# Performance work log

Hardware: AMD Instinct MI355X
Metric: run time of the kernel (lower is better)

The kernel has to match this reference:

```python
import jax, jax.numpy as jnp
import numpy as np

C = 256
NUM_HEADS = 8
NUM_GROUPS = 32
EPS = 1e-5


def setup_inputs() -> dict:
    key = jax.random.key(0)
    ks = jax.random.split(key, 7)
    B, H, W = 2, 64, 64
    x = jax.random.normal(ks[0], (B, C, H, W), dtype=jnp.float32)
    norm_gamma = jnp.ones((C,), dtype=jnp.float32)
    norm_beta = jnp.zeros((C,), dtype=jnp.float32)
    # 1x1 convs == per-pixel linear layers; store weights as (out_ch, in_ch)
    qkv_w = jax.random.normal(ks[1], (3 * C, C), dtype=jnp.float32) * (1.0 / np.sqrt(C))
    qkv_b = jnp.zeros((3 * C,), dtype=jnp.float32)
    proj_w = jax.random.normal(ks[2], (C, C), dtype=jnp.float32) * (1.0 / np.sqrt(C))
    proj_b = jnp.zeros((C,), dtype=jnp.float32)
    return {"x": x, "norm_gamma": norm_gamma, "norm_beta": norm_beta,
            "qkv_w": qkv_w, "qkv_b": qkv_b, "proj_w": proj_w, "proj_b": proj_b}


def _group_norm(x, gamma, beta):
    B, Cc, H, W = x.shape
    xg = x.reshape(B, NUM_GROUPS, Cc // NUM_GROUPS, H, W)
    mean = xg.mean(axis=(2, 3, 4), keepdims=True)
    var = xg.var(axis=(2, 3, 4), keepdims=True)
    xn = ((xg - mean) * jax.lax.rsqrt(var + EPS)).reshape(B, Cc, H, W)
    return xn * gamma[None, :, None, None] + beta[None, :, None, None]


def reference(x, norm_gamma, norm_beta, qkv_w, qkv_b, proj_w, proj_b):
    B, Cc, H, W = x.shape
    hd = Cc // NUM_HEADS
    N = H * W

    h = _group_norm(x, norm_gamma, norm_beta)
    # 1x1 conv: (3C,C) x (B,C,H,W) -> (B,3C,H,W)
    qkv = jnp.einsum('oc,bchw->bohw', qkv_w, h) + qkv_b[None, :, None, None]
    q, k, v = jnp.split(qkv, 3, axis=1)

    def heads(t):  # (B,C,H,W) -> (B,heads,N,hd)
        return t.reshape(B, NUM_HEADS, hd, N).transpose(0, 1, 3, 2)

    q, k, v = heads(q), heads(k), heads(v)
    scale = hd ** (-0.5)
    attn = jax.nn.softmax(jnp.einsum('bhnd,bhmd->bhnm', q, k) * scale, axis=-1)
    out = jnp.einsum('bhnm,bhmd->bhnd', attn, v)  # (B,heads,N,hd)
    out = out.transpose(0, 1, 3, 2).reshape(B, Cc, H, W)
    out = jnp.einsum('oc,bchw->bohw', proj_w, out) + proj_b[None, :, None, None]
    return x + out
```

## Files before the change

### kernel.cpp

```cpp
#include <hip/hip_runtime.h>
#include <math.h>

#define C_    256
#define NH    8
#define HD_   32
#define NG    32
#define CPG   8
#define NPIX  4096
#define BATCH 2
#define EPSV  1e-5f
#define SLOG2 0.25503489f
#define MF    16.0f
#define KVB   64
#define KSTR  40
#define VSTR  72
#define KPS2  2048

typedef __bf16 bf16x8 __attribute__((ext_vector_type(8)));
typedef __bf16 bf16x4 __attribute__((ext_vector_type(4)));
typedef float  f32x4  __attribute__((ext_vector_type(4)));

__global__ __launch_bounds__(256) void prep_kernel(const float* __restrict__ x,
                                                   float* __restrict__ stats,
                                                   const float* __restrict__ qw,
                                                   const float* __restrict__ pw,
                                                   __bf16* __restrict__ wbq,
                                                   __bf16* __restrict__ wbp) {
    if (blockIdx.x >= 64) {
        const int i = ((blockIdx.x - 64) * 256 + threadIdx.x) * 4;
        const float* src;
        __bf16* dst;
        int off;
        if (i < 768 * 256) { src = qw; dst = wbq; off = i; }
        else { src = pw; dst = wbp; off = i - 768 * 256; }
        const float4 v = *(const float4*)(src + off);
        bf16x4 o;
        o[0] = (__bf16)v.x; o[1] = (__bf16)v.y; o[2] = (__bf16)v.z; o[3] = (__bf16)v.w;
        *(bf16x4*)(dst + off) = o;
        return;
    }
    const int blk = blockIdx.x;
    const int b = blk >> 5, g = blk & 31;
    const float* __restrict__ xp = x + ((size_t)(b * C_ + g * CPG)) * NPIX;

    float s = 0.f, ss = 0.f;
    for (int i = threadIdx.x * 4; i < CPG * NPIX; i += 256 * 4) {
        const float4 v = *(const float4*)(xp + i);
        s  += v.x + v.y + v.z + v.w;
        ss += v.x * v.x + v.y * v.y + v.z * v.z + v.w * v.w;
    }
    #pragma unroll
    for (int off = 32; off; off >>= 1) {
        s  += __shfl_down(s, off);
        ss += __shfl_down(ss, off);
    }
    __shared__ float ls[4], lss[4];
    const int wid = threadIdx.x >> 6, lane = threadIdx.x & 63;
    if (lane == 0) { ls[wid] = s; lss[wid] = ss; }
    __syncthreads();
    if (threadIdx.x == 0) {
        float S = 0.f, SS = 0.f;
        #pragma unroll
        for (int w = 0; w < 4; ++w) { S += ls[w]; SS += lss[w]; }
        const float inv_n = 1.0f / (float)(CPG * NPIX);
        const float mean = S * inv_n;
        const float var  = SS * inv_n - mean * mean;
        stats[blk * 2 + 0] = mean;
        stats[blk * 2 + 1] = rsqrtf(var + EPSV);
    }
}

__global__ __launch_bounds__(256) void qkv_gemm_kernel(const __bf16* __restrict__ wbq,
                                                       const float* __restrict__ bias,
                                                       const float* __restrict__ x,
                                                       const float* __restrict__ stats,
                                                       const float* __restrict__ gamma,
                                                       const float* __restrict__ beta,
                                                       __bf16* __restrict__ Qb,
                                                       __bf16* __restrict__ Kb,
                                                       __bf16* __restrict__ Vb) {
    const int b = blockIdx.z;
    const int n0 = blockIdx.x * 32;
    __shared__ __align__(16) __bf16 tile[32][264];

    {
        const int nn = (threadIdx.x & 7) * 4;
        const int cb = threadIdx.x >> 3;
        #pragma unroll
        for (int p = 0; p < 8; ++p) {
            const int c = cb + p * 32;
            const float4 v = *(const float4*)(x + ((size_t)(b * C_ + c)) * NPIX + n0 + nn);
            const int g = c >> 3;
            const float mean = stats[(b * NG + g) * 2 + 0];
            const float rstd = stats[(b * NG + g) * 2 + 1];
            const float ga = gamma[c] * rstd;
            const float be = beta[c] - mean * ga;
            tile[nn + 0][c] = (__bf16)(v.x * ga + be);
            tile[nn + 1][c] = (__bf16)(v.y * ga + be);
            tile[nn + 2][c] = (__bf16)(v.z * ga + be);
            tile[nn + 3][c] = (__bf16)(v.w * ga + be);
        }
    }
    __syncthreads();

    const int wave = threadIdx.x >> 6, lane = threadIdx.x & 63;
    const int col = lane & 15, g = lane >> 4;
    const int m0 = blockIdx.y * 256 + wave * 64;

    f32x4 acc[4][2];
    #pragma unroll
    for (int i = 0; i < 4; ++i)
        #pragma unroll
        for (int j = 0; j < 2; ++j) acc[i][j] = (f32x4){0.f, 0.f, 0.f, 0.f};

    #pragma unroll
    for (int c0 = 0; c0 < C_; c0 += 32) {
        bf16x8 la[4], lb[2];
        #pragma unroll
        for (int mb = 0; mb < 4; ++mb)
            la[mb] = *(const bf16x8*)(wbq + (size_t)(m0 + mb * 16 + col) * C_ + c0 + g * 8);
        #pragma unroll
        for (int nb = 0; nb < 2; ++nb)
            lb[nb] = *(const bf16x8*)(&tile[nb * 16 + col][c0 + g * 8]);
        #pragma unroll
        for (int mb = 0; mb < 4; ++mb)
            #pragma unroll
            for (int nb = 0; nb < 2; ++nb)
                acc[mb][nb] = __builtin_amdgcn_mfma_f32_16x16x32_bf16(la[mb], lb[nb], acc[mb][nb], 0, 0, 0);
    }

    #pragma unroll
    for (int mb = 0; mb < 4; ++mb) {
        const int mbase = m0 + mb * 16 + 4 * g;
        const float4 b4 = *(const float4*)(bias + mbase);
        const int route = mbase >> 8;
        const int bh = b * NH + ((mbase >> 5) & 7);
        const int d0 = mbase & 31;
        #pragma unroll
        for (int nb = 0; nb < 2; ++nb) {
            const int n = n0 + nb * 16 + col;
            f32x4 v = acc[mb][nb];
            v[0] += b4.x; v[1] += b4.y; v[2] += b4.z; v[3] += b4.w;
            if (route == 0) {
                bf16x4 o;
                #pragma unroll
                for (int r = 0; r < 4; ++r) o[r] = (__bf16)(v[r] * SLOG2);
                *(bf16x4*)(Qb + (((size_t)bh * NPIX + n) << 5) + d0) = o;
            } else if (route == 1) {
                bf16x4 o;
                #pragma unroll
                for (int r = 0; r < 4; ++r) o[r] = (__bf16)v[r];
                *(bf16x4*)(Kb + (((size_t)bh * NPIX + n) << 5) + d0) = o;
            } else {
                #pragma unroll
                for (int r = 0; r < 4; ++r)
                    Vb[((size_t)bh * HD_ + d0 + r) * NPIX + n] = (__bf16)v[r];
            }
        }
    }
}

__global__ __launch_bounds__(512) void attn_kernel(const __bf16* __restrict__ Qb,
                                                   const __bf16* __restrict__ Kb,
                                                   const __bf16* __restrict__ Vb,
                                                   __bf16* __restrict__ aot) {
    __shared__ __align__(16) char smem[38912];
    __bf16 (*Ks)[2][KVB][KSTR] = (__bf16 (*)[2][KVB][KSTR])(smem);
    __bf16 (*Vs)[2][HD_][VSTR] = (__bf16 (*)[2][HD_][VSTR])(smem + 20480);
    float* pbuf = (float*)smem;

    const int id = blockIdx.x;
    const int h = id & 7;
    const int rest = id >> 3;
    const int b = rest >> 5;
    const int qt = rest & 31;

    const int wave = threadIdx.x >> 6, lane = threadIdx.x & 63;
    const int hw = wave >> 2, wv = wave & 3;
    const int col = lane & 15, g = lane >> 4;
    const int bh = b * NH + h;
    const int q0 = qt * 128 + wv * 32;

    const __bf16* __restrict__ qp = Qb + ((size_t)bh * NPIX + q0) * HD_;
    const __bf16* __restrict__ kp = Kb + ((size_t)bh * NPIX + hw * KPS2) * HD_;
    const __bf16* __restrict__ vp = Vb + (size_t)bh * HD_ * NPIX + hw * KPS2;

    const int sk_key = wv * 16 + (lane >> 2);
    const int sk_seg = (lane & 3) * 8;
    const int sv_d   = wv * 8 + (lane >> 3);
    const int sv_seg = (lane & 7) * 8;
    const int vslot  = (sv_seg & 32) + ((((sv_seg & 15) >> 2) << 3)) + (((sv_seg >> 4) & 1) << 2);
    const __bf16* __restrict__ kg = kp + (size_t)sk_key * HD_ + sk_seg;
    const __bf16* __restrict__ vg = vp + (size_t)sv_d * NPIX + sv_seg;

    const bf16x8 fq0 = *(const bf16x8*)(qp + col * HD_ + g * 8);
    const bf16x8 fq1 = *(const bf16x8*)(qp + (16 + col) * HD_ + g * 8);

    bf16x8 ones;
    #pragma unroll
    for (int j = 0; j < 8; ++j) ones[j] = (__bf16)1.0f;
    const f32x4 mfc = {-MF, -MF, -MF, -MF};

    f32x4 acc00 = {0.f,0.f,0.f,0.f}, acc01 = {0.f,0.f,0.f,0.f};
    f32x4 acc10 = {0.f,0.f,0.f,0.f}, acc11 = {0.f,0.f,0.f,0.f};
    f32x4 accL0 = {0.f,0.f,0.f,0.f}, accL1 = {0.f,0.f,0.f,0.f};

    {
        const bf16x8 rk = *(const bf16x8*)(kg);
        const bf16x8 rv = *(const bf16x8*)(vg);
        *(bf16x8*)&Ks[hw][0][sk_key][sk_seg] = rk;
        bf16x4 lo, hi;
        #pragma unroll
        for (int j = 0; j < 4; ++j) { lo[j] = rv[j]; hi[j] = rv[4 + j]; }
        *(bf16x4*)&Vs[hw][0][sv_d][vslot]     = lo;
        *(bf16x4*)&Vs[hw][0][sv_d][vslot + 8] = hi;
    }
    __syncthreads();

    const int nt = KPS2 / KVB;
    for (int t = 0; t < nt; ++t) {
        const int cur = t & 1;
        bf16x8 nk, nv;
        const bool more = (t + 1 < nt);
        {
            const size_t koff = (size_t)(more ? (t + 1) * KVB : 0);
            nk = *(const bf16x8*)(kg + koff * HD_);
            nv = *(const bf16x8*)(vg + koff);
        }

        #pragma unroll
        for (int kk = 0; kk < KVB; kk += 32) {
            const bf16x8 fk0 = *(const bf16x8*)(&Ks[hw][cur][kk + col][g * 8]);
            const bf16x8 fk1 = *(const bf16x8*)(&Ks[hw][cur][kk + 16 + col][g * 8]);
            const bf16x8 fv0 = *(const bf16x8*)(&Vs[hw][cur][col][kk + 8 * g]);
            const bf16x8 fv1 = *(const bf16x8*)(&Vs[hw][cur][col + 16][kk + 8 * g]);

            f32x4 s00 = __builtin_amdgcn_mfma_f32_16x16x32_bf16(fk0, fq0, mfc, 0, 0, 0);
            f32x4 s10 = __builtin_amdgcn_mfma_f32_16x16x32_bf16(fk1, fq0, mfc, 0, 0, 0);
            f32x4 s01 = __builtin_amdgcn_mfma_f32_16x16x32_bf16(fk0, fq1, mfc, 0, 0, 0);
            f32x4 s11 = __builtin_amdgcn_mfma_f32_16x16x32_bf16(fk1, fq1, mfc, 0, 0, 0);

            float p0[8], p1[8];
            #pragma unroll
            for (int r = 0; r < 4; ++r) {
                p0[r]     = __builtin_amdgcn_exp2f(s00[r]);
                p0[4 + r] = __builtin_amdgcn_exp2f(s10[r]);
                p1[r]     = __builtin_amdgcn_exp2f(s01[r]);
                p1[4 + r] = __builtin_amdgcn_exp2f(s11[r]);
            }

            bf16x8 fp0, fp1;
            #pragma unroll
            for (int j = 0; j < 8; ++j) { fp0[j] = (__bf16)p0[j]; fp1[j] = (__bf16)p1[j]; }

            accL0 = __builtin_amdgcn_mfma_f32_16x16x32_bf16(ones, fp0, accL0, 0, 0, 0);
            accL1 = __builtin_amdgcn_mfma_f32_16x16x32_bf16(ones, fp1, accL1, 0, 0, 0);
            acc00 = __builtin_amdgcn_mfma_f32_16x16x32_bf16(fv0, fp0, acc00, 0, 0, 0);
            acc01 = __builtin_amdgcn_mfma_f32_16x16x32_bf16(fv1, fp0, acc01, 0, 0, 0);
            acc10 = __builtin_amdgcn_mfma_f32_16x16x32_bf16(fv0, fp1, acc10, 0, 0, 0);
            acc11 = __builtin_amdgcn_mfma_f32_16x16x32_bf16(fv1, fp1, acc11, 0, 0, 0);
        }

        if (more) {
            *(bf16x8*)&Ks[hw][cur ^ 1][sk_key][sk_seg] = nk;
            bf16x4 lo, hi;
            #pragma unroll
            for (int j = 0; j < 4; ++j) { lo[j] = nv[j]; hi[j] = nv[4 + j]; }
            *(bf16x4*)&Vs[hw][cur ^ 1][sv_d][vslot]     = lo;
            *(bf16x4*)&Vs[hw][cur ^ 1][sv_d][vslot + 8] = hi;
        }
        __syncthreads();
    }

    float l0 = accL0[0], l1 = accL1[0];

    if (hw == 1) {
        float* pp = pbuf + ((size_t)wv * 64 + lane) * 20;
        *(f32x4*)(pp + 0)  = acc00;
        *(f32x4*)(pp + 4)  = acc01;
        *(f32x4*)(pp + 8)  = acc10;
        *(f32x4*)(pp + 12) = acc11;
        pp[16] = l0; pp[17] = l1;
    }
    __syncthreads();
    if (hw == 0) {
        const float* pp = pbuf + ((size_t)wv * 64 + lane) * 20;
        const f32x4 b00 = *(const f32x4*)(pp + 0);
        const f32x4 b01 = *(const f32x4*)(pp + 4);
        const f32x4 b10 = *(const f32x4*)(pp + 8);
        const f32x4 b11 = *(const f32x4*)(pp + 12);
        #pragma unroll
        for (int r = 0; r < 4; ++r) {
            acc00[r] += b00[r]; acc01[r] += b01[r];
            acc10[r] += b10[r]; acc11[r] += b11[r];
        }
        const float inv0 = 1.0f / (l0 + pp[16]);
        const float inv1 = 1.0f / (l1 + pp[17]);
        const int cb = h * HD_ + 4 * g;
        {
            __bf16* op = aot + ((size_t)(b * NPIX) + q0 + col) * C_ + cb;
            bf16x4 o0, o1;
            #pragma unroll
            for (int r = 0; r < 4; ++r) { o0[r] = (__bf16)(acc00[r] * inv0); o1[r] = (__bf16)(acc01[r] * inv0); }
            *(bf16x4*)(op) = o0;
            *(bf16x4*)(op + 16) = o1;
        }
        {
            __bf16* op = aot + ((size_t)(b * NPIX) + q0 + 16 + col) * C_ + cb;
            bf16x4 o0, o1;
            #pragma unroll
            for (int r = 0; r < 4; ++r) { o0[r] = (__bf16)(acc10[r] * inv1); o1[r] = (__bf16)(acc11[r] * inv1); }
            *(bf16x4*)(op) = o0;
            *(bf16x4*)(op + 16) = o1;
        }
    }
}

__global__ __launch_bounds__(256) void proj_gemm_kernel(const __bf16* __restrict__ wbp,
                                                        const float* __restrict__ bias,
                                                        const __bf16* __restrict__ aot,
                                                        const float* __restrict__ x,
                                                        float* __restrict__ out) {
    const int b = blockIdx.z;
    const int wave = threadIdx.x >> 6, lane = threadIdx.x & 63;
    const int col = lane & 15, g = lane >> 4;
    const int n0 = blockIdx.x * 64 + (wave & 1) * 32;
    const int m0 = blockIdx.y * 64 + (wave >> 1) * 32;
    const __bf16* __restrict__ ap = aot + (size_t)b * NPIX * C_;

    f32x4 acc[2][2];
    #pragma unroll
    for (int i = 0; i < 2; ++i)
        #pragma unroll
        for (int j = 0; j < 2; ++j) acc[i][j] = (f32x4){0.f, 0.f, 0.f, 0.f};

    #pragma unroll
    for (int c0 = 0; c0 < C_; c0 += 32) {
        bf16x8 la[2], lb[2];
        #pragma unroll
        for (int mb = 0; mb < 2; ++mb)
            la[mb] = *(const bf16x8*)(wbp + (size_t)(m0 + mb * 16 + col) * C_ + c0 + g * 8);
        #pragma unroll
        for (int nb = 0; nb < 2; ++nb)
            lb[nb] = *(const bf16x8*)(ap + (size_t)(n0 + nb * 16 + col) * C_ + c0 + g * 8);
        #pragma unroll
        for (int mb = 0; mb < 2; ++mb)
            #pragma unroll
            for (int nb = 0; nb < 2; ++nb)
                acc[mb][nb] = __builtin_amdgcn_mfma_f32_16x16x32_bf16(la[mb], lb[nb], acc[mb][nb], 0, 0, 0);
    }

    #pragma unroll
    for (int mb = 0; mb < 2; ++mb) {
        const int mbase = m0 + mb * 16 + 4 * g;
        const float4 b4 = *(const float4*)(bias + mbase);
        const float bias_r[4] = {b4.x, b4.y, b4.z, b4.w};
        #pragma unroll
        for (int nb = 0; nb < 2; ++nb) {
            const int n = n0 + nb * 16 + col;
            #pragma unroll
            for (int r = 0; r < 4; ++r) {
                const size_t idx = ((size_t)(b * C_ + mbase + r)) * NPIX + n;
                out[idx] = acc[mb][nb][r] + bias_r[r] + x[idx];
            }
        }
    }
}

extern "C" void kernel_launch(void* const* d_in, const int* in_sizes, int n_in,
                              void* d_out, int out_size, void* d_ws, size_t ws_size,
                              hipStream_t stream) {
    (void)in_sizes; (void)n_in; (void)out_size; (void)ws_size;
    const float* x      = (const float*)d_in[0];
    const float* gamma  = (const float*)d_in[1];
    const float* beta   = (const float*)d_in[2];
    const float* qkv_w  = (const float*)d_in[3];
    const float* qkv_b  = (const float*)d_in[4];
    const float* proj_w = (const float*)d_in[5];
    const float* proj_b = (const float*)d_in[6];
    float* out = (float*)d_out;

    char* ws = (char*)d_ws;
    __bf16* wbq  = (__bf16*)(ws);
    __bf16* wbp  = (__bf16*)(ws + 0x60000);
    float*  stats= (float*) (ws + 0x80000);
    __bf16* Qb   = (__bf16*)(ws + 0x500000);
    __bf16* Kb   = (__bf16*)(ws + 0x900000);
    __bf16* Vb   = (__bf16*)(ws + 0xD00000);
    __bf16* aot  = (__bf16*)(ws + 0x1100000);

    prep_kernel<<<dim3(320), dim3(256), 0, stream>>>(x, stats, qkv_w, proj_w, wbq, wbp);
    qkv_gemm_kernel<<<dim3(NPIX / 32, 3, BATCH), dim3(256), 0, stream>>>(
        wbq, qkv_b, x, stats, gamma, beta, Qb, Kb, Vb);
    attn_kernel<<<dim3(32 * NH * BATCH), dim3(512), 0, stream>>>(Qb, Kb, Vb, aot);
    proj_gemm_kernel<<<dim3(NPIX / 64, C_ / 64, BATCH), dim3(256), 0, stream>>>(wbp, proj_b, aot, x, out);
}
```

Before: 88.78 us.

## Enlarge attention KV tile to 128 and retile QKV GEMM to 128x64

The attention kernel now stages 128 keys/values per double-buffered step instead of 64, halving the number of loop iterations and block barriers, with each thread loading two K and two V segments per step. Shared memory grows to about 74 KB per block, which may limit occupancy to one block per CU. The QKV GEMM block tile changes from 256 output channels by 32 pixels to 128 channels by 64 pixels. Each wave now computes a 32x64 sub-tile, which changes the balance between weight reuse and normalized-input reuse, and the grid shape changes accordingly.

```diff
diff --git a/kernel.cpp b/kernel.cpp
--- a/kernel.cpp
+++ b/kernel.cpp
@@ -11,9 +11,9 @@
 #define EPSV  1e-5f
 #define SLOG2 0.25503489f
 #define MF    16.0f
-#define KVB   64
+#define KVB   128
 #define KSTR  40
-#define VSTR  72
+#define VSTR  136
 #define KPS2  2048
 
 typedef __bf16 bf16x8 __attribute__((ext_vector_type(8)));
@@ -80,15 +80,14 @@
                                                        __bf16* __restrict__ Kb,
                                                        __bf16* __restrict__ Vb) {
     const int b = blockIdx.z;
-    const int n0 = blockIdx.x * 32;
-    __shared__ __align__(16) __bf16 tile[32][264];
+    const int n0 = blockIdx.x * 64;
+    __shared__ __align__(16) __bf16 tile[64][264];
 
     {
-        const int nn = (threadIdx.x & 7) * 4;
-        const int cb = threadIdx.x >> 3;
-        #pragma unroll
-        for (int p = 0; p < 8; ++p) {
-            const int c = cb + p * 32;
+        const int nn = (threadIdx.x & 15) * 4;
+        #pragma unroll
+        for (int p = 0; p < 16; ++p) {
+            const int c = (threadIdx.x >> 4) + p * 16;
             const float4 v = *(const float4*)(x + ((size_t)(b * C_ + c)) * NPIX + n0 + nn);
             const int g = c >> 3;
             const float mean = stats[(b * NG + g) * 2 + 0];
@@ -105,39 +104,39 @@
 
     const int wave = threadIdx.x >> 6, lane = threadIdx.x & 63;
     const int col = lane & 15, g = lane >> 4;
-    const int m0 = blockIdx.y * 256 + wave * 64;
-
-    f32x4 acc[4][2];
-    #pragma unroll
-    for (int i = 0; i < 4; ++i)
-        #pragma unroll
-        for (int j = 0; j < 2; ++j) acc[i][j] = (f32x4){0.f, 0.f, 0.f, 0.f};
+    const int m0 = blockIdx.y * 128 + wave * 32;
+
+    f32x4 acc[2][4];
+    #pragma unroll
+    for (int i = 0; i < 2; ++i)
+        #pragma unroll
+        for (int j = 0; j < 4; ++j) acc[i][j] = (f32x4){0.f, 0.f, 0.f, 0.f};
 
     #pragma unroll
     for (int c0 = 0; c0 < C_; c0 += 32) {
-        bf16x8 la[4], lb[2];
-        #pragma unroll
-        for (int mb = 0; mb < 4; ++mb)
+        bf16x8 la[2], lb[4];
+        #pragma unroll
+        for (int mb = 0; mb < 2; ++mb)
             la[mb] = *(const bf16x8*)(wbq + (size_t)(m0 + mb * 16 + col) * C_ + c0 + g * 8);
         #pragma unroll
-        for (int nb = 0; nb < 2; ++nb)
+        for (int nb = 0; nb < 4; ++nb)
             lb[nb] = *(const bf16x8*)(&tile[nb * 16 + col][c0 + g * 8]);
         #pragma unroll
-        for (int mb = 0; mb < 4; ++mb)
-            #pragma unroll
-            for (int nb = 0; nb < 2; ++nb)
+        for (int mb = 0; mb < 2; ++mb)
+            #pragma unroll
+            for (int nb = 0; nb < 4; ++nb)
                 acc[mb][nb] = __builtin_amdgcn_mfma_f32_16x16x32_bf16(la[mb], lb[nb], acc[mb][nb], 0, 0, 0);
     }
 
     #pragma unroll
-    for (int mb = 0; mb < 4; ++mb) {
+    for (int mb = 0; mb < 2; ++mb) {
         const int mbase = m0 + mb * 16 + 4 * g;
         const float4 b4 = *(const float4*)(bias + mbase);
         const int route = mbase >> 8;
         const int bh = b * NH + ((mbase >> 5) & 7);
         const int d0 = mbase & 31;
         #pragma unroll
-        for (int nb = 0; nb < 2; ++nb) {
+        for (int nb = 0; nb < 4; ++nb) {
             const int n = n0 + nb * 16 + col;
             f32x4 v = acc[mb][nb];
             v[0] += b4.x; v[1] += b4.y; v[2] += b4.z; v[3] += b4.w;
@@ -164,9 +163,9 @@
                                                    const __bf16* __restrict__ Kb,
                                                    const __bf16* __restrict__ Vb,
                                                    __bf16* __restrict__ aot) {
-    __shared__ __align__(16) char smem[38912];
+    __shared__ __align__(16) char smem[75776];
     __bf16 (*Ks)[2][KVB][KSTR] = (__bf16 (*)[2][KVB][KSTR])(smem);
-    __bf16 (*Vs)[2][HD_][VSTR] = (__bf16 (*)[2][HD_][VSTR])(smem + 20480);
+    __bf16 (*Vs)[2][HD_][VSTR] = (__bf16 (*)[2][HD_][VSTR])(smem + 40960);
     float* pbuf = (float*)smem;
 
     const int id = blockIdx.x;
@@ -206,26 +205,35 @@
     f32x4 accL0 = {0.f,0.f,0.f,0.f}, accL1 = {0.f,0.f,0.f,0.f};
 
     {
-        const bf16x8 rk = *(const bf16x8*)(kg);
-        const bf16x8 rv = *(const bf16x8*)(vg);
-        *(bf16x8*)&Ks[hw][0][sk_key][sk_seg] = rk;
+        const bf16x8 rk0 = *(const bf16x8*)(kg);
+        const bf16x8 rk1 = *(const bf16x8*)(kg + (size_t)64 * HD_);
+        const bf16x8 rv0 = *(const bf16x8*)(vg);
+        const bf16x8 rv1 = *(const bf16x8*)(vg + 64);
+        *(bf16x8*)&Ks[hw][0][sk_key][sk_seg]      = rk0;
+        *(bf16x8*)&Ks[hw][0][sk_key + 64][sk_seg] = rk1;
         bf16x4 lo, hi;
         #pragma unroll
-        for (int j = 0; j < 4; ++j) { lo[j] = rv[j]; hi[j] = rv[4 + j]; }
+        for (int j = 0; j < 4; ++j) { lo[j] = rv0[j]; hi[j] = rv0[4 + j]; }
         *(bf16x4*)&Vs[hw][0][sv_d][vslot]     = lo;
         *(bf16x4*)&Vs[hw][0][sv_d][vslot + 8] = hi;
+        #pragma unroll
+        for (int j = 0; j < 4; ++j) { lo[j] = rv1[j]; hi[j] = rv1[4 + j]; }
+        *(bf16x4*)&Vs[hw][0][sv_d][vslot + 64]     = lo;
+        *(bf16x4*)&Vs[hw][0][sv_d][vslot + 64 + 8] = hi;
     }
     __syncthreads();
 
     const int nt = KPS2 / KVB;
     for (int t = 0; t < nt; ++t) {
         const int cur = t & 1;
-        bf16x8 nk, nv;
+        bf16x8 nk0, nk1, nv0, nv1;
         const bool more = (t + 1 < nt);
         {
             const size_t koff = (size_t)(more ? (t + 1) * KVB : 0);
-            nk = *(const bf16x8*)(kg + koff * HD_);
-            nv = *(const bf16x8*)(vg + koff);
+            nk0 = *(const bf16x8*)(kg + koff * HD_);
+            nk1 = *(const bf16x8*)(kg + (koff + 64) * HD_);
+            nv0 = *(const bf16x8*)(vg + koff);
+            nv1 = *(const bf16x8*)(vg + koff + 64);
         }
 
         #pragma unroll
@@ -262,12 +270,17 @@
         }
 
         if (more) {
-            *(bf16x8*)&Ks[hw][cur ^ 1][sk_key][sk_seg] = nk;
+            *(bf16x8*)&Ks[hw][cur ^ 1][sk_key][sk_seg]      = nk0;
+            *(bf16x8*)&Ks[hw][cur ^ 1][sk_key + 64][sk_seg] = nk1;
             bf16x4 lo, hi;
             #pragma unroll
-            for (int j = 0; j < 4; ++j) { lo[j] = nv[j]; hi[j] = nv[4 + j]; }
+            for (int j = 0; j < 4; ++j) { lo[j] = nv0[j]; hi[j] = nv0[4 + j]; }
             *(bf16x4*)&Vs[hw][cur ^ 1][sv_d][vslot]     = lo;
             *(bf16x4*)&Vs[hw][cur ^ 1][sv_d][vslot + 8] = hi;
+            #pragma unroll
+            for (int j = 0; j < 4; ++j) { lo[j] = nv1[j]; hi[j] = nv1[4 + j]; }
+            *(bf16x4*)&Vs[hw][cur ^ 1][sv_d][vslot + 64]     = lo;
+            *(bf16x4*)&Vs[hw][cur ^ 1][sv_d][vslot + 64 + 8] = hi;
         }
         __syncthreads();
     }
@@ -390,7 +403,7 @@
     __bf16* aot  = (__bf16*)(ws + 0x1100000);
 
     prep_kernel<<<dim3(320), dim3(256), 0, stream>>>(x, stats, qkv_w, proj_w, wbq, wbp);
-    qkv_gemm_kernel<<<dim3(NPIX / 32, 3, BATCH), dim3(256), 0, stream>>>(
+    qkv_gemm_kernel<<<dim3(NPIX / 64, 768 / 128, BATCH), dim3(256), 0, stream>>>(
         wbq, qkv_b, x, stats, gamma, beta, Qb, Kb, Vb);
     attn_kernel<<<dim3(32 * NH * BATCH), dim3(512), 0, stream>>>(Qb, Kb, Vb, aot);
     proj_gemm_kernel<<<dim3(NPIX / 64, C_ / 64, BATCH), dim3(256), 0, stream>>>(wbp, proj_b, aot, x, out);
```

Result: faster. 84.90 us (-4.4%).
